# Kernel tuning notes

Hardware: AMD Instinct MI355X
Metric: run time of the kernel (lower is better)

## Reference

```python
import jax, jax.numpy as jnp
import numpy as np

N_NODES = 50000
N_EDGES = 800000
F_IN = 32
HID = 64
K = 4  # Chebyshev order in GConvLSTM(node_features, hidden, 4)


def setup_inputs() -> dict:
    key = jax.random.key(0)
    ks = jax.random.split(key, 14)
    x = jax.random.normal(ks[0], (N_NODES, F_IN), dtype=jnp.float32)
    edge_index = jax.random.randint(ks[1], (2, N_EDGES), 0, N_NODES, dtype=jnp.int64)
    edge_weight = jax.random.uniform(ks[2], (N_EDGES,), dtype=jnp.float32)
    s = 0.05
    # gate order: i, f, c, o
    Wx = jax.random.normal(ks[3], (4, K, F_IN, HID), dtype=jnp.float32) * s  # ChebConv weights on x
    bx = jax.random.normal(ks[4], (4, HID), dtype=jnp.float32) * s          # ChebConv biases on x
    Wh = jax.random.normal(ks[5], (4, K, HID, HID), dtype=jnp.float32) * s  # ChebConv weights on h
    bh = jax.random.normal(ks[6], (4, HID), dtype=jnp.float32) * s          # ChebConv biases on h
    wc = jax.random.normal(ks[7], (3, HID), dtype=jnp.float32) * s          # peephole w_c_i, w_c_f, w_c_o
    bg = jax.random.normal(ks[8], (4, HID), dtype=jnp.float32) * s          # gate biases b_i, b_f, b_c, b_o
    lin_w = jax.random.normal(ks[9], (HID, 1), dtype=jnp.float32) * s
    lin_b = jax.random.normal(ks[10], (1,), dtype=jnp.float32) * s
    return {"x": x, "edge_index": edge_index, "edge_weight": edge_weight,
            "Wx": Wx, "bx": bx, "Wh": Wh, "bh": bh, "wc": wc, "bg": bg,
            "lin_w": lin_w, "lin_b": lin_b}


def _cheb_norm(edge_index, edge_weight, num_nodes):
    # ChebConv.__norm__, sym normalization, lambda_max=2.0:
    # L_hat off-diagonal = -D^{-1/2} A D^{-1/2}, diagonal = 0.
    src, dst = edge_index[0], edge_index[1]
    deg = jax.ops.segment_sum(edge_weight, src, num_segments=num_nodes)
    d_inv_sqrt = jnp.where(deg > 0, jax.lax.rsqrt(jnp.maximum(deg, 1e-30)), 0.0)
    norm = -d_inv_sqrt[src] * edge_weight * d_inv_sqrt[dst]
    return src, dst, norm


def _cheb_conv(v, src, dst, norm, W, b, num_nodes):
    # ChebConv forward: out = sum_k T_k(L_hat) v @ W[k] + b, with propagate
    # = segment_sum of norm * v[src] at dst.
    def prop(t):
        return jax.ops.segment_sum(norm[:, None] * t[src], dst, num_segments=num_nodes)
    Tx0 = v
    out = Tx0 @ W[0]
    Tx1 = prop(Tx0)
    out = out + Tx1 @ W[1]
    for k in range(2, W.shape[0]):
        Tx2 = 2.0 * prop(Tx1) - Tx0
        out = out + Tx2 @ W[k]
        Tx0, Tx1 = Tx1, Tx2
    return out + b


def reference(x, edge_index, edge_weight, Wx, bx, Wh, bh, wc, bg, lin_w, lin_b):
    N = x.shape[0]
    src, dst, norm = _cheb_norm(edge_index, edge_weight, N)
    H = jnp.zeros((N, Wh.shape[-1]), dtype=x.dtype)
    C = jnp.zeros((N, Wh.shape[-1]), dtype=x.dtype)

    def gate(g, v_state):
        return (_cheb_conv(x, src, dst, norm, Wx[g], bx[g], N)
                + _cheb_conv(v_state, src, dst, norm, Wh[g], bh[g], N))

    I = jax.nn.sigmoid(gate(0, H) + wc[0] * C + bg[0])
    F = jax.nn.sigmoid(gate(1, H) + wc[1] * C + bg[1])
    T = jnp.tanh(gate(2, H) + bg[2])
    C = F * C + I * T
    O = jax.nn.sigmoid(gate(3, H) + wc[2] * C + bg[3])
    H = O * jnp.tanh(C)
    # dropout(p=0.25) is identity at inference; linear head HID -> 1
    return H @ lin_w + lin_b
```

## Files before the change

### kernel.cpp

```cpp
#include <hip/hip_runtime.h>
#include <math.h>


#define NT 256
#define NCH 64
#define RSD 25600
#define RSF 20480

typedef __attribute__((ext_vector_type(8))) short short8v;
typedef __attribute__((ext_vector_type(8))) unsigned short ushort8v;
typedef __attribute__((ext_vector_type(4))) float f32x4;

__device__ __forceinline__ short f2bf(float f) {
    unsigned u = __float_as_uint(f);
    u += 0x7FFFu + ((u >> 16) & 1u);
    return (short)(u >> 16);
}
__device__ __forceinline__ float bf2f(unsigned short b) {
    return __uint_as_float((unsigned)b << 16);
}

__global__ __launch_bounds__(1024)
void k_front(const int* __restrict__ src, const int* __restrict__ dst,
             const float* __restrict__ w, float* __restrict__ degPart,
             unsigned short* __restrict__ cntPart,
             const float* __restrict__ Wx, short* __restrict__ P,
             const float* __restrict__ x, short* __restrict__ xb,
             int nE, int N, int degB, int n4) {
    __shared__ unsigned smem[RSD];
    const int bid = blockIdx.x;
    const int chunk = (nE + NCH - 1) / NCH;

    if (bid < degB) {
        float* s_deg = reinterpret_cast<float*>(smem);
        const int r = bid / NCH, b = bid % NCH;
        const int base = r * RSD;
        for (int i = threadIdx.x; i < RSD; i += 1024) s_deg[i] = 0.f;
        __syncthreads();
        const int e0 = b * chunk, e1 = min(e0 + chunk, nE);
        for (int e = e0 + (int)threadIdx.x; e < e1; e += 1024) {
            unsigned so = (unsigned)(src[e] - base);
            if (so < RSD) atomicAdd(&s_deg[so], w[e]);
        }
        __syncthreads();
        const int lim = min(RSD, N - base);
        for (int i = threadIdx.x; i < lim; i += 1024)
            degPart[(size_t)b * N + base + i] = s_deg[i];
        return;
    }
    if (bid < degB + NCH) {
        unsigned* s_cnt2 = smem;
        const int b = bid - degB;
        const int pairsN = (N + 1) >> 1;
        for (int i = threadIdx.x; i < pairsN; i += 1024) s_cnt2[i] = 0u;
        __syncthreads();
        const int e0 = b * chunk, e1 = min(e0 + chunk, nE);
        for (int e = e0 + (int)threadIdx.x; e < e1; e += 1024) {
            unsigned d = (unsigned)dst[e];
            atomicAdd(&s_cnt2[d >> 1], 1u << ((d & 1) * 16));
        }
        __syncthreads();
        unsigned* cp32 = reinterpret_cast<unsigned*>(cntPart + (size_t)b * N);
        for (int i = threadIdx.x; i < pairsN; i += 1024) cp32[i] = s_cnt2[i];
        return;
    }
    int idx = (bid - degB - NCH) * 1024 + (int)threadIdx.x;
    if (idx < 12 * 4 * 64) {
        int lane = idx & 63;
        int kt = (idx >> 6) & 3;
        int nt = idx >> 8;
        int gate = (nt < 4) ? 0 : (nt < 8) ? 2 : 3;
        int h = (nt & 3) * 16 + (lane & 15);
        int fb = (lane >> 4) * 8;
        short8v v;
#pragma unroll
        for (int j = 0; j < 8; ++j)
            v[j] = f2bf(Wx[((size_t)(gate * 4 + kt) * 32 + fb + j) * 64 + h]);
        *(reinterpret_cast<short8v*>(P) + idx) = v;
        return;
    }
    int i = idx - 12 * 4 * 64;
    if (i >= n4) return;
    const float4 v = *reinterpret_cast<const float4*>(x + (size_t)i * 4);
    short4 rb;
    rb.x = f2bf(v.x); rb.y = f2bf(v.y); rb.z = f2bf(v.z); rb.w = f2bf(v.w);
    *reinterpret_cast<short4*>(xb + (size_t)i * 4) = rb;
}

__global__ __launch_bounds__(NT)
void k_scan_merged(const float* __restrict__ degPart,
                   const unsigned short* __restrict__ cntPart,
                   float* __restrict__ dinv, int* __restrict__ cnt,
                   int* __restrict__ rowptr, int* __restrict__ partials,
                   int* __restrict__ flag, int* __restrict__ offs, int N) {
    __shared__ unsigned s_c[NCH * NT];
    __shared__ int sp[NT];
    const int t = threadIdx.x;
    const int n0 = blockIdx.x * (NT * 2) + t * 2;
    float d0 = 0.f, d1 = 0.f;
    int c0 = 0, c1 = 0;
    if (n0 < N) {
#pragma unroll 8
        for (int b = 0; b < NCH; ++b) {
            const float2 dv = *reinterpret_cast<const float2*>(degPart + (size_t)b * N + n0);
            d0 += dv.x; d1 += dv.y;
            unsigned cc = *reinterpret_cast<const unsigned*>(cntPart + (size_t)b * N + n0);
            s_c[b * NT + t] = cc;
            c0 += (int)(cc & 0xFFFFu); c1 += (int)(cc >> 16);
        }
        dinv[n0] = d0 > 0.f ? rsqrtf(d0) : 0.f;
        cnt[n0] = c0;
        if (n0 + 1 < N) {
            dinv[n0 + 1] = d1 > 0.f ? rsqrtf(d1) : 0.f;
            cnt[n0 + 1] = c1;
        } else c1 = 0;
    }
    int cs = c0 + c1;
    sp[t] = cs;
    __syncthreads();
    for (int off = 1; off < NT; off <<= 1) {
        int u = (t >= off) ? sp[t - off] : 0;
        __syncthreads();
        sp[t] += u;
        __syncthreads();
    }
    const int ex = sp[t] - cs;
    const int total = sp[NT - 1];
    __syncthreads();
    if (t == 0) {
        __hip_atomic_store(&partials[blockIdx.x], total, __ATOMIC_RELEASE,
                           __HIP_MEMORY_SCOPE_AGENT);
        atomicAdd(flag, 1);
        while (__hip_atomic_load(flag, __ATOMIC_ACQUIRE,
                                 __HIP_MEMORY_SCOPE_AGENT) < (int)gridDim.x)
            __builtin_amdgcn_s_sleep(1);
    }
    __syncthreads();
    int v = (t < (int)blockIdx.x)
                ? __hip_atomic_load(&partials[t], __ATOMIC_ACQUIRE,
                                    __HIP_MEMORY_SCOPE_AGENT)
                : 0;
    sp[t] = v;
    __syncthreads();
    for (int off = NT / 2; off > 0; off >>= 1) {
        if (t < off) sp[t] += sp[t + off];
        __syncthreads();
    }
    const int prefix = sp[0];
    if (n0 >= N) return;
    const bool has1 = (n0 + 1) < N;
    int s0 = ex + prefix;
    int s1 = has1 ? ex + c0 + prefix : 0;
    rowptr[n0] = s0;
    if (has1) rowptr[n0 + 1] = s1;
#pragma unroll 8
    for (int b = 0; b < NCH; ++b) {
        unsigned cc = s_c[b * NT + t];
        if (has1) {
            *reinterpret_cast<int2*>(offs + (size_t)b * N + n0) = make_int2(s0, s1);
        } else {
            offs[(size_t)b * N + n0] = s0;
        }
        s0 += (int)(cc & 0xFFFFu);
        s1 += (int)(cc >> 16);
    }
}

__global__ __launch_bounds__(1024)
void k_fill2(const int* __restrict__ src, const int* __restrict__ dst,
             const float* __restrict__ w, const float* __restrict__ dinv,
             const int* __restrict__ offs, int2* __restrict__ entries,
             int nE, int N) {
    __shared__ int s_cur[RSF];
    const int r = blockIdx.x / NCH, b = blockIdx.x % NCH;
    const int base = r * RSF;
    const int lim = min(RSF, N - base);
    for (int i = threadIdx.x; i < lim; i += 1024)
        s_cur[i] = offs[(size_t)b * N + base + i];
    __syncthreads();
    const int chunk = (nE + NCH - 1) / NCH;
    const int e0 = b * chunk, e1 = min(e0 + chunk, nE);
    for (int e = e0 + (int)threadIdx.x; e < e1; e += 1024) {
        int d = dst[e];
        unsigned dof = (unsigned)(d - base);
        if (dof < RSF) {
            int s = src[e];
            float nv = -dinv[s] * w[e] * dinv[d];
            int pos = atomicAdd(&s_cur[dof], 1);
            entries[pos] = make_int2(s, __float_as_int(nv));
        }
    }
}

__device__ __forceinline__ void bf8_fma(float* acc, ushort8v v, float s) {
#pragma unroll
    for (int j = 0; j < 8; ++j)
        acc[j] = fmaf(s, bf2f(v[j]), acc[j]);
}

__global__ __launch_bounds__(256)
void k_gather_bf(const unsigned short* __restrict__ tb,
                 const unsigned short* __restrict__ subb,
                 short* __restrict__ outb,
                 const int* __restrict__ rowptr, const int* __restrict__ cnt,
                 const int2* __restrict__ entries, float scale, int N) {
    int idx = blockIdx.x * blockDim.x + threadIdx.x;
    if (idx >= N * 16) return;
    int n = idx >> 4, tq = idx & 3, qr = (idx >> 2) & 3;
    int beg = rowptr[n], end = beg + cnt[n];
    float acc0[8] = {0, 0, 0, 0, 0, 0, 0, 0};
    float acc1[8] = {0, 0, 0, 0, 0, 0, 0, 0};
    int i = beg + qr;
    for (; i + 12 < end; i += 16) {
        int2 e0 = entries[i];
        int2 e1 = entries[i + 4];
        int2 e2 = entries[i + 8];
        int2 e3 = entries[i + 12];
        ushort8v v0 = *reinterpret_cast<const ushort8v*>(tb + (size_t)e0.x * 32 + tq * 8);
        ushort8v v1 = *reinterpret_cast<const ushort8v*>(tb + (size_t)e1.x * 32 + tq * 8);
        ushort8v v2 = *reinterpret_cast<const ushort8v*>(tb + (size_t)e2.x * 32 + tq * 8);
        ushort8v v3 = *reinterpret_cast<const ushort8v*>(tb + (size_t)e3.x * 32 + tq * 8);
        bf8_fma(acc0, v0, __int_as_float(e0.y));
        bf8_fma(acc1, v1, __int_as_float(e1.y));
        bf8_fma(acc0, v2, __int_as_float(e2.y));
        bf8_fma(acc1, v3, __int_as_float(e3.y));
    }
    for (; i < end; i += 4) {
        int2 e0 = entries[i];
        ushort8v v0 = *reinterpret_cast<const ushort8v*>(tb + (size_t)e0.x * 32 + tq * 8);
        bf8_fma(acc0, v0, __int_as_float(e0.y));
    }
    float r[8];
#pragma unroll
    for (int j = 0; j < 8; ++j) {
        r[j] = acc0[j] + acc1[j];
        r[j] += __shfl_xor(r[j], 4);
        r[j] += __shfl_xor(r[j], 8);
    }
    if (qr == 0) {
        if (subb) {
            ushort8v sv = *reinterpret_cast<const ushort8v*>(subb + (size_t)n * 32 + tq * 8);
#pragma unroll
            for (int j = 0; j < 8; ++j) r[j] = fmaf(scale, r[j], -bf2f(sv[j]));
        } else {
#pragma unroll
            for (int j = 0; j < 8; ++j) r[j] *= scale;
        }
        short8v rb;
#pragma unroll
        for (int j = 0; j < 8; ++j) rb[j] = f2bf(r[j]);
        *reinterpret_cast<short8v*>(outb + (size_t)n * 32 + tq * 8) = rb;
    }
}

__device__ __forceinline__ float sigf(float x) {
    return __builtin_amdgcn_rcpf(1.f + __builtin_amdgcn_exp2f(-1.4426950408889634f * x));
}
__device__ __forceinline__ float tanhf_fast(float x) {
    float e = __builtin_amdgcn_exp2f(2.8853900817779268f * x);
    return 1.f - 2.f * __builtin_amdgcn_rcpf(e + 1.f);
}

__global__ __launch_bounds__(256)
void k_final_g3(const short* __restrict__ xb, const short* __restrict__ t1b,
                const unsigned short* __restrict__ t2b,
                const short* __restrict__ P,
                const int* __restrict__ rowptr, const int* __restrict__ cnt,
                const int2* __restrict__ entries,
                const float* __restrict__ bx, const float* __restrict__ bh,
                const float* __restrict__ wc, const float* __restrict__ bg,
                const float* __restrict__ lin_w, const float* __restrict__ lin_b,
                float* __restrict__ out, int N) {
    const int wave = threadIdx.x >> 6, lane = threadIdx.x & 63;
    const int nb = blockIdx.x * 64 + wave * 16;
    const int rc = min(nb + (lane & 15), N - 1);
    const int ko = (lane >> 4) * 8;

    int beg = rowptr[rc], end = beg + cnt[rc];
    float acc0[8] = {0, 0, 0, 0, 0, 0, 0, 0};
    float acc1[8] = {0, 0, 0, 0, 0, 0, 0, 0};
    int i = beg;
    for (; i + 3 < end; i += 4) {
        int2 e0 = entries[i];
        int2 e1 = entries[i + 1];
        int2 e2 = entries[i + 2];
        int2 e3 = entries[i + 3];
        ushort8v v0 = *reinterpret_cast<const ushort8v*>(t2b + (size_t)e0.x * 32 + ko);
        ushort8v v1 = *reinterpret_cast<const ushort8v*>(t2b + (size_t)e1.x * 32 + ko);
        ushort8v v2 = *reinterpret_cast<const ushort8v*>(t2b + (size_t)e2.x * 32 + ko);
        ushort8v v3 = *reinterpret_cast<const ushort8v*>(t2b + (size_t)e3.x * 32 + ko);
        bf8_fma(acc0, v0, __int_as_float(e0.y));
        bf8_fma(acc1, v1, __int_as_float(e1.y));
        bf8_fma(acc0, v2, __int_as_float(e2.y));
        bf8_fma(acc1, v3, __int_as_float(e3.y));
    }
    for (; i < end; ++i) {
        int2 e0 = entries[i];
        ushort8v v0 = *reinterpret_cast<const ushort8v*>(t2b + (size_t)e0.x * 32 + ko);
        bf8_fma(acc0, v0, __int_as_float(e0.y));
    }

    short8v A0 = *reinterpret_cast<const short8v*>(xb  + (size_t)rc * 32 + ko);
    short8v A1 = *reinterpret_cast<const short8v*>(t1b + (size_t)rc * 32 + ko);
    short8v A2 = *reinterpret_cast<const short8v*>(
        reinterpret_cast<const short*>(t2b) + (size_t)rc * 32 + ko);
    short8v A3;
#pragma unroll
    for (int j = 0; j < 8; ++j)
        A3[j] = f2bf(2.f * (acc0[j] + acc1[j]) - bf2f((unsigned short)A1[j]));

    const short8v* Pv = reinterpret_cast<const short8v*>(P);
    f32x4 acc[12];
#pragma unroll
    for (int nt = 0; nt < 12; ++nt) {
        const short8v* Pb = Pv + (size_t)nt * 4 * 64 + lane;
        f32x4 a = {0.f, 0.f, 0.f, 0.f};
        a = __builtin_amdgcn_mfma_f32_16x16x32_bf16(A0, Pb[0],   a, 0, 0, 0);
        a = __builtin_amdgcn_mfma_f32_16x16x32_bf16(A1, Pb[64],  a, 0, 0, 0);
        a = __builtin_amdgcn_mfma_f32_16x16x32_bf16(A2, Pb[128], a, 0, 0, 0);
        a = __builtin_amdgcn_mfma_f32_16x16x32_bf16(A3, Pb[192], a, 0, 0, 0);
        acc[nt] = a;
    }

    const int hq = lane & 15;
    const int ng = lane >> 4;
    const float lb = lin_b[0];
    float p[4] = {0.f, 0.f, 0.f, 0.f};
#pragma unroll
    for (int ht = 0; ht < 4; ++ht) {
        int h = ht * 16 + hq;
        float bI = bx[h] + bh[h] + bg[h];
        float bC = bx[128 + h] + bh[128 + h] + bg[128 + h];
        float bO = bx[192 + h] + bh[192 + h] + bg[192 + h];
        float w2 = wc[128 + h];
        float lw = lin_w[h];
#pragma unroll
        for (int r = 0; r < 4; ++r) {
            float I = sigf(acc[ht][r] + bI);
            float T = tanhf_fast(acc[4 + ht][r] + bC);
            float C = I * T;
            float O = sigf(acc[8 + ht][r] + bO + w2 * C);
            float H = O * tanhf_fast(C);
            p[r] = fmaf(H, lw, p[r]);
        }
    }
#pragma unroll
    for (int r = 0; r < 4; ++r) {
        float v = p[r];
        v += __shfl_xor(v, 1);
        v += __shfl_xor(v, 2);
        v += __shfl_xor(v, 4);
        v += __shfl_xor(v, 8);
        if (hq == 0) {
            int n = nb + ng * 4 + r;
            if (n < N) out[n] = v + lb;
        }
    }
}

extern "C" void kernel_launch(void* const* d_in, const int* in_sizes, int n_in,
                              void* d_out, int out_size, void* d_ws, size_t ws_size,
                              hipStream_t stream) {
    const float* x   = (const float*)d_in[0];
    const int*   ei  = (const int*)d_in[1];
    const float* ew  = (const float*)d_in[2];
    const float* Wx  = (const float*)d_in[3];
    const float* bx  = (const float*)d_in[4];
    const float* bh  = (const float*)d_in[6];
    const float* wcp = (const float*)d_in[7];
    const float* bg  = (const float*)d_in[8];
    const float* lw  = (const float*)d_in[9];
    const float* lb  = (const float*)d_in[10];
    float* out = (float*)d_out;

    const int N  = in_sizes[0] / 32;
    const int nE = in_sizes[2];
    const int* src = ei;
    const int* dst = ei + nE;

    char* ws = (char*)d_ws;
    size_t off = 0;
    float* dinv    = (float*)(ws + off); off += (size_t)N * 4;
    int*   cnt     = (int*)(ws + off);   off += (size_t)N * 4;
    int*   rowptr  = (int*)(ws + off);   off += (size_t)N * 4;
    int*   partials= (int*)(ws + off);   off += 1024 * 4;
    int*   flag    = (int*)(ws + off);   off += 256;
    short* P       = (short*)(ws + off); off += 12 * 4 * 64 * 8 * 2;
    int2*  entries = (int2*)(ws + off);  off += (size_t)nE * 8;
    float* degPart = (float*)(ws + off); off += (size_t)NCH * N * 4;
    unsigned short* cntPart = (unsigned short*)(ws + off); off += (size_t)NCH * N * 2;
    short* xbuf    = (short*)(ws + off); off += (size_t)N * 32 * 2;
    short* Tx1b    = (short*)(ws + off); off += (size_t)N * 32 * 2;
    short* Tx2b    = (short*)(ws + off); off += (size_t)N * 32 * 2;

    int* offs = (int*)degPart;

    const int nRangeD = (N + RSD - 1) / RSD;
    const int degB = nRangeD * NCH;
    const int n4 = N * 8;
    const int xbB = (12 * 4 * 64 + n4 + 1023) / 1024;
    const int nb2 = (N + NT * 2 - 1) / (NT * 2);
    const int nRangeF = (N + RSF - 1) / RSF;

    hipMemsetAsync(flag, 0, 4, stream);
    k_front<<<degB + NCH + xbB, 1024, 0, stream>>>(src, dst, ew, degPart, cntPart,
                                                   Wx, P, x, xbuf, nE, N, degB, n4);
    k_scan_merged<<<nb2, NT, 0, stream>>>(degPart, cntPart, dinv, cnt, rowptr,
                                          partials, flag, offs, N);
    k_fill2<<<nRangeF * NCH, 1024, 0, stream>>>(src, dst, ew, dinv, offs,
                                                entries, nE, N);

    const int gb = (N * 16 + NT - 1) / NT;
    k_gather_bf<<<gb, NT, 0, stream>>>((const unsigned short*)xbuf, nullptr,
                                       Tx1b, rowptr, cnt, entries, 1.f, N);
    k_gather_bf<<<gb, NT, 0, stream>>>((const unsigned short*)Tx1b,
                                       (const unsigned short*)xbuf,
                                       Tx2b, rowptr, cnt, entries, 2.f, N);

    const int fb = (N + 63) / 64;
    k_final_g3<<<fb, NT, 0, stream>>>(xbuf, Tx1b, (const unsigned short*)Tx2b, P,
                                      rowptr, cnt, entries, bx, bh, wcp, bg,
                                      lw, lb, out, N);
}
```

Baseline: 104.4 us.

## Fuse two gather passes into one persistent kernel with grid barrier

The two back-to-back gather launches become a single persistent kernel of 2048 blocks that runs both Chebyshev propagation steps, separated by a software grid-wide barrier on an atomic flag. The flag reset moves from a memset into the first kernel, which removes one API call. The scan kernel's spin-wait switches to relaxed polling with a longer sleep followed by an acquire fence. The goal is to cut launch overhead and inter-kernel gaps, at the cost of needing every block to be co-resident for the barrier and of running the gather with a grid-stride loop.

```diff
diff --git a/kernel.cpp b/kernel.cpp
--- a/kernel.cpp
+++ b/kernel.cpp
@@ -6,6 +6,8 @@
 #define NCH 64
 #define RSD 25600
 #define RSF 20480
+#define G12 2048
+#define NT12 256
 
 typedef __attribute__((ext_vector_type(8))) short short8v;
 typedef __attribute__((ext_vector_type(8))) unsigned short ushort8v;
@@ -18,6 +20,18 @@
 }
 __device__ __forceinline__ float bf2f(unsigned short b) {
     return __uint_as_float((unsigned)b << 16);
+}
+
+__device__ __forceinline__ void gbar(int* flag, int target) {
+    __syncthreads();
+    if (threadIdx.x == 0) {
+        __hip_atomic_fetch_add(flag, 1, __ATOMIC_RELEASE, __HIP_MEMORY_SCOPE_AGENT);
+        while (__hip_atomic_load(flag, __ATOMIC_RELAXED,
+                                 __HIP_MEMORY_SCOPE_AGENT) < target)
+            __builtin_amdgcn_s_sleep(8);
+        __builtin_amdgcn_fence(__ATOMIC_ACQUIRE, "agent");
+    }
+    __syncthreads();
 }
 
 __global__ __launch_bounds__(1024)
@@ -26,10 +40,11 @@
              unsigned short* __restrict__ cntPart,
              const float* __restrict__ Wx, short* __restrict__ P,
              const float* __restrict__ x, short* __restrict__ xb,
-             int nE, int N, int degB, int n4) {
+             int* __restrict__ flags, int nE, int N, int degB, int n4) {
     __shared__ unsigned smem[RSD];
     const int bid = blockIdx.x;
     const int chunk = (nE + NCH - 1) / NCH;
+    if (bid == 0 && threadIdx.x < 2) flags[threadIdx.x] = 0;
 
     if (bid < degB) {
         float* s_deg = reinterpret_cast<float*>(smem);
@@ -130,14 +145,15 @@
     if (t == 0) {
         __hip_atomic_store(&partials[blockIdx.x], total, __ATOMIC_RELEASE,
                            __HIP_MEMORY_SCOPE_AGENT);
-        atomicAdd(flag, 1);
-        while (__hip_atomic_load(flag, __ATOMIC_ACQUIRE,
+        __hip_atomic_fetch_add(flag, 1, __ATOMIC_RELEASE, __HIP_MEMORY_SCOPE_AGENT);
+        while (__hip_atomic_load(flag, __ATOMIC_RELAXED,
                                  __HIP_MEMORY_SCOPE_AGENT) < (int)gridDim.x)
-            __builtin_amdgcn_s_sleep(1);
+            __builtin_amdgcn_s_sleep(8);
+        __builtin_amdgcn_fence(__ATOMIC_ACQUIRE, "agent");
     }
     __syncthreads();
     int v = (t < (int)blockIdx.x)
-                ? __hip_atomic_load(&partials[t], __ATOMIC_ACQUIRE,
+                ? __hip_atomic_load(&partials[t], __ATOMIC_RELAXED,
                                     __HIP_MEMORY_SCOPE_AGENT)
                 : 0;
     sp[t] = v;
@@ -198,14 +214,11 @@
         acc[j] = fmaf(s, bf2f(v[j]), acc[j]);
 }
 
-__global__ __launch_bounds__(256)
-void k_gather_bf(const unsigned short* __restrict__ tb,
-                 const unsigned short* __restrict__ subb,
-                 short* __restrict__ outb,
-                 const int* __restrict__ rowptr, const int* __restrict__ cnt,
-                 const int2* __restrict__ entries, float scale, int N) {
-    int idx = blockIdx.x * blockDim.x + threadIdx.x;
-    if (idx >= N * 16) return;
+__device__ __forceinline__ void gather_item(
+    const unsigned short* __restrict__ tb, const unsigned short* __restrict__ subb,
+    short* __restrict__ outb, const int* __restrict__ rowptr,
+    const int* __restrict__ cnt, const int2* __restrict__ entries,
+    float scale, int idx) {
     int n = idx >> 4, tq = idx & 3, qr = (idx >> 2) & 3;
     int beg = rowptr[n], end = beg + cnt[n];
     float acc0[8] = {0, 0, 0, 0, 0, 0, 0, 0};
@@ -253,6 +266,23 @@
     }
 }
 
+__global__ __launch_bounds__(NT12, 8)
+void k_gather12(const short* __restrict__ xb, short* __restrict__ Tx1b,
+                short* __restrict__ Tx2b,
+                const int* __restrict__ rowptr, const int* __restrict__ cnt,
+                const int2* __restrict__ entries, int* __restrict__ flag, int N) {
+    const int stride = G12 * NT12;
+    const int tid0 = blockIdx.x * NT12 + (int)threadIdx.x;
+    const unsigned short* xbu = reinterpret_cast<const unsigned short*>(xb);
+
+    for (int idx = tid0; idx < N * 16; idx += stride)
+        gather_item(xbu, nullptr, Tx1b, rowptr, cnt, entries, 1.f, idx);
+    gbar(flag, G12);
+    for (int idx = tid0; idx < N * 16; idx += stride)
+        gather_item(reinterpret_cast<const unsigned short*>(Tx1b), xbu, Tx2b,
+                    rowptr, cnt, entries, 2.f, idx);
+}
+
 __device__ __forceinline__ float sigf(float x) {
     return __builtin_amdgcn_rcpf(1.f + __builtin_amdgcn_exp2f(-1.4426950408889634f * x));
 }
@@ -384,7 +414,7 @@
     int*   cnt     = (int*)(ws + off);   off += (size_t)N * 4;
     int*   rowptr  = (int*)(ws + off);   off += (size_t)N * 4;
     int*   partials= (int*)(ws + off);   off += 1024 * 4;
-    int*   flag    = (int*)(ws + off);   off += 256;
+    int*   flags   = (int*)(ws + off);   off += 256;
     short* P       = (short*)(ws + off); off += 12 * 4 * 64 * 8 * 2;
     int2*  entries = (int2*)(ws + off);  off += (size_t)nE * 8;
     float* degPart = (float*)(ws + off); off += (size_t)NCH * N * 4;
@@ -402,21 +432,15 @@
     const int nb2 = (N + NT * 2 - 1) / (NT * 2);
     const int nRangeF = (N + RSF - 1) / RSF;
 
-    hipMemsetAsync(flag, 0, 4, stream);
     k_front<<<degB + NCH + xbB, 1024, 0, stream>>>(src, dst, ew, degPart, cntPart,
-                                                   Wx, P, x, xbuf, nE, N, degB, n4);
+                                                   Wx, P, x, xbuf, flags,
+                                                   nE, N, degB, n4);
     k_scan_merged<<<nb2, NT, 0, stream>>>(degPart, cntPart, dinv, cnt, rowptr,
-                                          partials, flag, offs, N);
+                                          partials, &flags[0], offs, N);
     k_fill2<<<nRangeF * NCH, 1024, 0, stream>>>(src, dst, ew, dinv, offs,
                                                 entries, nE, N);
-
-    const int gb = (N * 16 + NT - 1) / NT;
-    k_gather_bf<<<gb, NT, 0, stream>>>((const unsigned short*)xbuf, nullptr,
-                                       Tx1b, rowptr, cnt, entries, 1.f, N);
-    k_gather_bf<<<gb, NT, 0, stream>>>((const unsigned short*)Tx1b,
-                                       (const unsigned short*)xbuf,
-                                       Tx2b, rowptr, cnt, entries, 2.f, N);
-
+    k_gather12<<<G12, NT12, 0, stream>>>(xbuf, Tx1b, Tx2b, rowptr, cnt, entries,
+                                         &flags[1], N);
     const int fb = (N + 63) / 64;
     k_final_g3<<<fb, NT, 0, stream>>>(xbuf, Tx1b, (const unsigned short*)Tx2b, P,
                                       rowptr, cnt, entries, bx, bh, wcp, bg,
```

Result: slower. 308.6 us (+195.7%).
